# Optimization experiments

Measured on AMD Instinct MI355X. Metric: run time of the kernel, lower is better.

Reference implementation:

```python
import jax, jax.numpy as jnp
import numpy as np

N, C, H, W = 512, 512, 14, 14
CH, CW = 7, 7  # RoIAlign crop size


def conv1x1(x, w, b):
    # x: [N,C,H,W], w: [O,C], b: [O]  (1x1 conv == channel GEMM)
    return jnp.einsum('nchw,oc->nohw', x, w) + b[None, :, None, None]


def roi_align_fpcoor(x, boxes, ch, cw):
    """RoIAlign(transform_fpcoor=True) as in longcw/RoIAlign.pytorch.
    x: [N,C,H,W]; boxes: [N,4] = (x1,y1,x2,y2) in feature-pixel coords,
    box n crops image n. Returns [N,C,ch,cw]."""
    Hf, Wf = x.shape[2], x.shape[3]
    x1, y1, x2, y2 = boxes[:, 0], boxes[:, 1], boxes[:, 2], boxes[:, 3]
    sw = (x2 - x1) / cw
    sh = (y2 - y1) / ch
    nx0 = (x1 + sw * 0.5 - 0.5) / (Wf - 1)
    ny0 = (y1 + sh * 0.5 - 0.5) / (Hf - 1)
    nw = sw * (cw - 1) / (Wf - 1)
    nh = sh * (ch - 1) / (Hf - 1)
    # tf.crop_and_resize sample coordinates (crop size > 1 branch)
    ys = ny0[:, None] * (Hf - 1) + jnp.arange(ch, dtype=x.dtype) * (nh[:, None] * (Hf - 1) / (ch - 1))  # [N,ch]
    xs = nx0[:, None] * (Wf - 1) + jnp.arange(cw, dtype=x.dtype) * (nw[:, None] * (Wf - 1) / (cw - 1))  # [N,cw]
    y0f = jnp.floor(ys); x0f = jnp.floor(xs)
    wy = (ys - y0f)[:, :, None, None]          # [N,ch,1,1]
    wx = (xs - x0f)[:, None, :, None]          # [N,1,cw,1]
    y0 = jnp.clip(y0f.astype(jnp.int32), 0, Hf - 1)
    y1i = jnp.clip(y0 + 1, 0, Hf - 1)
    x0 = jnp.clip(x0f.astype(jnp.int32), 0, Wf - 1)
    x1i = jnp.clip(x0 + 1, 0, Wf - 1)
    b = jnp.arange(x.shape[0])[:, None, None]  # [N,1,1]
    yA = y0[:, :, None]; yB = y1i[:, :, None]  # [N,ch,1]
    xA = x0[:, None, :]; xB = x1i[:, None, :]  # [N,1,cw]
    # advanced indexing -> [N,ch,cw,C]
    v00 = x[b, :, yA, xA]; v01 = x[b, :, yA, xB]
    v10 = x[b, :, yB, xA]; v11 = x[b, :, yB, xB]
    top = v00 + (v01 - v00) * wx
    bot = v10 + (v11 - v10) * wx
    out = top + (bot - top) * wy               # [N,ch,cw,C]
    return jnp.transpose(out, (0, 3, 1, 2))    # [N,C,ch,cw]


def setup_inputs() -> dict:
    key = jax.random.key(0)
    ks = jax.random.split(key, 11)
    s = 0.02
    d = C * CH * CW  # 512*49
    return {
        'project': jax.random.normal(ks[0], (N, C, H, W), jnp.float32),
        'w1': jax.random.normal(ks[1], (C, C), jnp.float32) * s,
        'b1': jnp.zeros((C,), jnp.float32),
        'w2': jax.random.normal(ks[2], (C, C), jnp.float32) * s,
        'b2': jnp.zeros((C,), jnp.float32),
        'w3': jax.random.normal(ks[3], (C, C), jnp.float32) * s,
        'b3': jnp.zeros((C,), jnp.float32),
        'w_note': jax.random.normal(ks[4], (2, d), jnp.float32) * s,
        'b_note': jnp.zeros((2,), jnp.float32),
        'w_reg': jax.random.normal(ks[5], (8, d), jnp.float32) * s,
        'b_reg': jnp.zeros((8,), jnp.float32),
    }


def reference(project, w1, b1, w2, b2, w3, b3, w_note, b_note, w_reg, b_reg):
    x = conv1x1(project, w1, b1)
    x = conv1x1(x, w2, b2)
    # boxes are a fixed constant inside forward: [0,0,13,13] per RoI
    boxes = jnp.tile(jnp.asarray([[0.0, 0.0, 13.0, 13.0]], jnp.float32), (project.shape[0], 1))
    x = roi_align_fpcoor(x, boxes, CH, CW)     # [N,512,7,7]
    x = conv1x1(x, w3, b3)
    x = x.reshape((-1, C * CH * CW))
    note = x @ w_note.T + b_note
    reg = x @ w_reg.T + b_reg
    return note, reg
```

## Files before the change

### kernel.cpp

```cpp
#include <hip/hip_runtime.h>


#define CHW4 25088
#define STEP 1.8571428571428572f

__global__ __launch_bounds__(512) void k_prep1(
    const float* __restrict__ w_note, const float* __restrict__ w_reg,
    const float* __restrict__ w2, const float* __restrict__ b1,
    const float* __restrict__ b2,
    float* __restrict__ WH, float* __restrict__ u2) {
    int blk = blockIdx.x;
    int tid = threadIdx.x;
    if (blk < 490) {
        int k = blk / 49, ji = blk % 49;
        const float* wh = (k < 2) ? (w_note + k * 25088) : (w_reg + (k - 2) * 25088);
        WH[(size_t)blk * 512 + tid] = wh[tid * 49 + ji];
    } else {
        int wv = tid >> 6, lane = tid & 63;
        int o = (blk - 490) * 8 + wv;
        float s = 0.f;
        #pragma unroll
        for (int r = 0; r < 8; ++r) s += w2[(size_t)o * 512 + lane + r * 64] * b1[lane + r * 64];
        for (int off = 32; off; off >>= 1) s += __shfl_down(s, off);
        if (lane == 0) u2[o] = b2[o] + s;
    }
}

__global__ __launch_bounds__(256) void k_prep2(
    const float* __restrict__ w1, const float* __restrict__ w2,
    const float* __restrict__ w3, const float* __restrict__ WH,
    const float* __restrict__ u2, const float* __restrict__ b3,
    float* __restrict__ Y, float* __restrict__ T1, float* __restrict__ vv) {
    int blk = blockIdx.x;
    int tid = threadIdx.x;
    if (blk < 512) {
        __shared__ float As[32][36];
        __shared__ float Bs[32][36];
        const float* A; const float* B; float* C; int M;
        if (blk < 256) { A = w2; B = w1; C = Y;  M = 512; }
        else           { A = WH; B = w3; C = T1; M = 490; }
        int t = blk & 255;
        int bx = t & 15, by = t >> 4;
        int lr = tid >> 3, lc = (tid & 7) << 2;
        int tx = tid & 15, ty = tid >> 4;
        float a00 = 0.f, a01 = 0.f, a10 = 0.f, a11 = 0.f;
        for (int kc = 0; kc < 512; kc += 32) {
            int gr = by * 32 + lr;
            float4 av = make_float4(0.f, 0.f, 0.f, 0.f);
            if (gr < M) av = *(const float4*)&A[(size_t)gr * 512 + kc + lc];
            *(float4*)&As[lr][lc] = av;
            *(float4*)&Bs[lr][lc] = *(const float4*)&B[(size_t)(kc + lr) * 512 + bx * 32 + lc];
            __syncthreads();
            #pragma unroll
            for (int kk = 0; kk < 32; ++kk) {
                float b0 = Bs[kk][tx * 2], b1v = Bs[kk][tx * 2 + 1];
                float x0 = As[ty * 2][kk], x1 = As[ty * 2 + 1][kk];
                a00 += x0 * b0; a01 += x0 * b1v;
                a10 += x1 * b0; a11 += x1 * b1v;
            }
            __syncthreads();
        }
        int r0 = by * 32 + ty * 2, c0 = bx * 32 + tx * 2;
        if (r0 < M)     { C[(size_t)r0 * 512 + c0] = a00; C[(size_t)r0 * 512 + c0 + 1] = a01; }
        if (r0 + 1 < M) { C[(size_t)(r0 + 1) * 512 + c0] = a10; C[(size_t)(r0 + 1) * 512 + c0 + 1] = a11; }
    } else {
        int wv = tid >> 6, lane = tid & 63;
        int o = (blk - 512) * 4 + wv;
        float s = 0.f;
        #pragma unroll
        for (int r = 0; r < 8; ++r) s += w3[(size_t)o * 512 + lane + r * 64] * u2[lane + r * 64];
        for (int off = 32; off; off >>= 1) s += __shfl_down(s, off);
        if (lane == 0) vv[o] = b3[o] + s;
    }
}

__global__ __launch_bounds__(256) void k_prep3(
    const float* __restrict__ T1, const float* __restrict__ Y,
    const float* __restrict__ w_note, const float* __restrict__ w_reg,
    const float* __restrict__ vv,
    float* __restrict__ Bt, float* __restrict__ dpart) {
    int blk = blockIdx.x;
    int tid = threadIdx.x;
    if (blk < 256) {
        __shared__ float As[32][36];
        __shared__ float Bs[32][36];
        int bx = blk & 15, by = blk >> 4;
        int lr = tid >> 3, lc = (tid & 7) << 2;
        int tx = tid & 15, ty = tid >> 4;
        int gr = by * 32 + lr;
        float a00 = 0.f, a01 = 0.f, a10 = 0.f, a11 = 0.f;
        for (int kc = 0; kc < 512; kc += 32) {
            float4 av = make_float4(0.f, 0.f, 0.f, 0.f);
            if (gr < 490) av = *(const float4*)&T1[(size_t)gr * 512 + kc + lc];
            *(float4*)&As[lr][lc] = av;
            *(float4*)&Bs[lr][lc] = *(const float4*)&Y[(size_t)(kc + lr) * 512 + bx * 32 + lc];
            __syncthreads();
            #pragma unroll
            for (int kk = 0; kk < 32; ++kk) {
                float b0 = Bs[kk][tx * 2], b1v = Bs[kk][tx * 2 + 1];
                float x0 = As[ty * 2][kk], x1 = As[ty * 2 + 1][kk];
                a00 += x0 * b0; a01 += x0 * b1v;
                a10 += x1 * b0; a11 += x1 * b1v;
            }
            __syncthreads();
        }
        int r0 = by * 32 + ty * 2, c0 = bx * 32 + tx * 2;
        if (r0 < 490) {
            int k = r0 / 49, ji = r0 - k * 49;
            Bt[((size_t)(ji * 512 + c0)) * 12 + k] = a00;
            Bt[((size_t)(ji * 512 + c0 + 1)) * 12 + k] = a01;
        }
        if (r0 + 1 < 490) {
            int k = (r0 + 1) / 49, ji = (r0 + 1) - k * 49;
            Bt[((size_t)(ji * 512 + c0)) * 12 + k] = a10;
            Bt[((size_t)(ji * 512 + c0 + 1)) * 12 + k] = a11;
        }
    } else {
        int t = blk - 256;
        int k = t >> 3, b8 = t & 7;
        const float* wh = (k < 2) ? (w_note + k * 25088) : (w_reg + (k - 2) * 25088);
        float s = 0.f;
        for (int i = b8 * 256 + tid; i < 25088; i += 2048) s += wh[i] * vv[i / 49];
        __shared__ float red[256];
        red[tid] = s;
        __syncthreads();
        for (int off = 128; off; off >>= 1) {
            if (tid < off) red[tid] += red[tid + off];
            __syncthreads();
        }
        if (tid == 0) dpart[k * 8 + b8] = red[0];
    }
}

__global__ __launch_bounds__(256) void k_mainf(const float* __restrict__ proj,
                                               const float* __restrict__ Bt,
                                               float* __restrict__ part) {
    __shared__ float X[2][16][197];
    int b = blockIdx.x;
    int n = b >> 1;
    int ch0 = (b & 1) << 4;
    int tid = threadIdx.x;
    int wv = tid >> 6, lane = tid & 63;

    int cc0 = tid / 49,            q0 = tid - (tid / 49) * 49;
    int cc1 = cc0 + 5,             q1 = q0 + 11; if (q1 >= 49) { q1 -= 49; ++cc1; }
    int cc2 = cc1 + 5,             q2 = q1 + 11; if (q2 >= 49) { q2 -= 49; ++cc2; }

    const float base = STEP * 0.5f - 0.5f;
    int   i00s[4];
    float wxs[4], wys[4];
    size_t boff[4];
    #pragma unroll
    for (int s = 0; s < 4; ++s) {
        int o = tid + s * 256;
        if (o > 783) o = 783;
        int ji = o >> 4, cl = o & 15;
        int j = (ji * 37) >> 8;
        int i2 = ji - j * 7;
        float yv = base + j * STEP;
        float xv = base + i2 * STEP;
        float y0f = floorf(yv), x0f = floorf(xv);
        wys[s] = yv - y0f; wxs[s] = xv - x0f;
        i00s[s] = cl * 197 + (int)y0f * 14 + (int)x0f;
        boff[s] = ((size_t)(ji << 9) + (ch0 << 4) + cl) * 12;
    }

    const float4* src0 = (const float4*)proj + (size_t)n * CHW4 + ch0 * 784;
    float acc[10];
    #pragma unroll
    for (int k = 0; k < 10; ++k) acc[k] = 0.f;

    {
        float4 v0 = src0[tid];
        float4 v1 = src0[tid + 256];
        float4 v2 = src0[tid + 512];
        float* xb = &X[0][0][0];
        *(float4*)&xb[cc0 * 197 + q0 * 4] = v0;
        *(float4*)&xb[cc1 * 197 + q1 * 4] = v1;
        *(float4*)&xb[cc2 * 197 + q2 * 4] = v2;
        if (tid < 16) *(float4*)&xb[15 * 197 + (tid + 33) * 4] = src0[tid + 768];
    }
    __syncthreads();

    int cur = 0;
    #pragma unroll 1
    for (int t = 0; t < 16; ++t) {
        float4 v0, v1, v2, v3;
        if (t < 15) {
            const float4* sn = src0 + (t + 1) * 784;
            v0 = sn[tid]; v1 = sn[tid + 256]; v2 = sn[tid + 512];
            if (tid < 16) v3 = sn[tid + 768];
        }
        const float* xb = &X[cur][0][0];
        size_t tof = (size_t)t * 192;
        #pragma unroll
        for (int s = 0; s < 3; ++s) {
            int i00 = i00s[s];
            float v00 = xb[i00],      v01 = xb[i00 + 1];
            float v10 = xb[i00 + 14], v11 = xb[i00 + 15];
            float top = v00 + (v01 - v00) * wxs[s];
            float bot = v10 + (v11 - v10) * wxs[s];
            float v = top + (bot - top) * wys[s];
            const float* bp = Bt + boff[s] + tof;
            float4 c0 = *(const float4*)bp;
            float4 c1 = *(const float4*)(bp + 4);
            float2 c2 = *(const float2*)(bp + 8);
            acc[0] += v * c0.x; acc[1] += v * c0.y; acc[2] += v * c0.z; acc[3] += v * c0.w;
            acc[4] += v * c1.x; acc[5] += v * c1.y; acc[6] += v * c1.z; acc[7] += v * c1.w;
            acc[8] += v * c2.x; acc[9] += v * c2.y;
        }
        if (tid < 16) {
            int i00 = i00s[3];
            float v00 = xb[i00],      v01 = xb[i00 + 1];
            float v10 = xb[i00 + 14], v11 = xb[i00 + 15];
            float top = v00 + (v01 - v00) * wxs[3];
            float bot = v10 + (v11 - v10) * wxs[3];
            float v = top + (bot - top) * wys[3];
            const float* bp = Bt + boff[3] + tof;
            float4 c0 = *(const float4*)bp;
            float4 c1 = *(const float4*)(bp + 4);
            float2 c2 = *(const float2*)(bp + 8);
            acc[0] += v * c0.x; acc[1] += v * c0.y; acc[2] += v * c0.z; acc[3] += v * c0.w;
            acc[4] += v * c1.x; acc[5] += v * c1.y; acc[6] += v * c1.z; acc[7] += v * c1.w;
            acc[8] += v * c2.x; acc[9] += v * c2.y;
        }
        if (t < 15) {
            float* xw = &X[cur ^ 1][0][0];
            *(float4*)&xw[cc0 * 197 + q0 * 4] = v0;
            *(float4*)&xw[cc1 * 197 + q1 * 4] = v1;
            *(float4*)&xw[cc2 * 197 + q2 * 4] = v2;
            if (tid < 16) *(float4*)&xw[15 * 197 + (tid + 33) * 4] = v3;
        }
        __syncthreads();
        cur ^= 1;
    }

    #pragma unroll
    for (int k = 0; k < 10; ++k) {
        float v = acc[k];
        v += __shfl_xor(v, 1);
        v += __shfl_xor(v, 2);
        v += __shfl_xor(v, 4);
        v += __shfl_xor(v, 8);
        v += __shfl_xor(v, 16);
        v += __shfl_xor(v, 32);
        if (lane == k) part[((size_t)b * 4 + wv) * 10 + k] = v;
    }
}

__global__ void k_reduce(const float* __restrict__ part,
                         const float* __restrict__ dpart,
                         const float* __restrict__ b_note, const float* __restrict__ b_reg,
                         float* __restrict__ out) {
    int idx = blockIdx.x * 256 + threadIdx.x;
    int n = idx / 10, k = idx % 10;
    float s = (k < 2) ? b_note[k] : b_reg[k - 2];
    for (int b = 0; b < 8; ++b) s += dpart[k * 8 + b];
    #pragma unroll
    for (int h = 0; h < 2; ++h)
        for (int w = 0; w < 4; ++w)
            s += part[(((size_t)(n * 2 + h)) * 4 + w) * 10 + k];
    if (k < 2) out[n * 2 + k] = s;
    else       out[1024 + n * 8 + (k - 2)] = s;
}

extern "C" void kernel_launch(void* const* d_in, const int* in_sizes, int n_in,
                              void* d_out, int out_size, void* d_ws, size_t ws_size,
                              hipStream_t stream) {
    const float* proj   = (const float*)d_in[0];
    const float* w1     = (const float*)d_in[1];
    const float* b1     = (const float*)d_in[2];
    const float* w2     = (const float*)d_in[3];
    const float* b2     = (const float*)d_in[4];
    const float* w3     = (const float*)d_in[5];
    const float* b3     = (const float*)d_in[6];
    const float* w_note = (const float*)d_in[7];
    const float* b_note = (const float*)d_in[8];
    const float* w_reg  = (const float*)d_in[9];
    const float* b_reg  = (const float*)d_in[10];

    float* ws    = (float*)d_ws;
    float* WH    = ws;
    float* Y     = WH + 250880;
    float* T1    = Y + 262144;
    float* Bt    = T1 + 250880;
    float* u2    = Bt + 301056;
    float* vv    = u2 + 512;
    float* dpart = vv + 512;
    float* part  = dpart + 80;
    float* out   = (float*)d_out;

    k_prep1<<<554, 512, 0, stream>>>(w_note, w_reg, w2, b1, b2, WH, u2);
    k_prep2<<<640, 256, 0, stream>>>(w1, w2, w3, WH, u2, b3, Y, T1, vv);
    k_prep3<<<336, 256, 0, stream>>>(T1, Y, w_note, w_reg, vv, Bt, dpart);
    k_mainf<<<1024, 256, 0, stream>>>(proj, Bt, part);
    k_reduce<<<20, 256, 0, stream>>>(part, dpart, b_note, b_reg, out);
}
```

Measured before the change: 100.2 us.

## Give each wavefront its own 4-channel LDS tile and drop block barriers

Each of the four wavefronts now loads, stores to LDS and consumes its own 4-channel slice of the input, so no cross-wave sharing exists and the per-iteration __syncthreads is removed. Bt loads for all slots are issued at the top of each iteration, ahead of the next-tile prefetch, with a sched_barrier to fix that ordering and hide latency. This trades block-level synchronization for per-wave independence. It relies on LDS writes and reads within a wavefront being ordered without an explicit barrier, and it loads 12 floats per Bt slot where only 10 are used.

```diff
diff --git a/kernel.cpp b/kernel.cpp
--- a/kernel.cpp
+++ b/kernel.cpp
@@ -135,105 +135,106 @@
 __global__ __launch_bounds__(256) void k_mainf(const float* __restrict__ proj,
                                                const float* __restrict__ Bt,
                                                float* __restrict__ part) {
-    __shared__ float X[2][16][197];
+    __shared__ float X[4][2][788];
     int b = blockIdx.x;
     int n = b >> 1;
     int ch0 = (b & 1) << 4;
     int tid = threadIdx.x;
     int wv = tid >> 6, lane = tid & 63;
 
-    int cc0 = tid / 49,            q0 = tid - (tid / 49) * 49;
-    int cc1 = cc0 + 5,             q1 = q0 + 11; if (q1 >= 49) { q1 -= 49; ++cc1; }
-    int cc2 = cc1 + 5,             q2 = q1 + 11; if (q2 >= 49) { q2 -= 49; ++cc2; }
+    int cc0 = lane / 49, q0 = lane - cc0 * 49;
+    int cc1 = cc0 + 1, q1 = q0 + 15; if (q1 >= 49) { q1 -= 49; ++cc1; }
+    int cc2 = cc1 + 1, q2 = q1 + 15; if (q2 >= 49) { q2 -= 49; ++cc2; }
+    bool l4 = lane < 4;
+    int q3 = 45 + lane;
 
     const float base = STEP * 0.5f - 0.5f;
-    int   i00s[4];
+    int i00s[4], boffs[4];
     float wxs[4], wys[4];
-    size_t boff[4];
     #pragma unroll
     for (int s = 0; s < 4; ++s) {
-        int o = tid + s * 256;
-        if (o > 783) o = 783;
-        int ji = o >> 4, cl = o & 15;
+        int o = s * 64 + lane; if (o > 195) o = 195;
+        int ji = o >> 2, cl4 = o & 3;
         int j = (ji * 37) >> 8;
         int i2 = ji - j * 7;
         float yv = base + j * STEP;
         float xv = base + i2 * STEP;
         float y0f = floorf(yv), x0f = floorf(xv);
         wys[s] = yv - y0f; wxs[s] = xv - x0f;
-        i00s[s] = cl * 197 + (int)y0f * 14 + (int)x0f;
-        boff[s] = ((size_t)(ji << 9) + (ch0 << 4) + cl) * 12;
-    }
-
-    const float4* src0 = (const float4*)proj + (size_t)n * CHW4 + ch0 * 784;
+        i00s[s] = cl4 * 197 + (int)y0f * 14 + (int)x0f;
+        boffs[s] = ((ji << 9) + (ch0 << 4) + (wv << 2) + cl4) * 12;
+    }
+
+    const float4* srcb = (const float4*)proj + (size_t)n * CHW4 + ch0 * 784 + wv * 196;
     float acc[10];
     #pragma unroll
     for (int k = 0; k < 10; ++k) acc[k] = 0.f;
 
+    float4 v0, v1, v2, v3;
     {
-        float4 v0 = src0[tid];
-        float4 v1 = src0[tid + 256];
-        float4 v2 = src0[tid + 512];
-        float* xb = &X[0][0][0];
-        *(float4*)&xb[cc0 * 197 + q0 * 4] = v0;
-        *(float4*)&xb[cc1 * 197 + q1 * 4] = v1;
-        *(float4*)&xb[cc2 * 197 + q2 * 4] = v2;
-        if (tid < 16) *(float4*)&xb[15 * 197 + (tid + 33) * 4] = src0[tid + 768];
-    }
-    __syncthreads();
-
-    int cur = 0;
+        v0 = srcb[lane]; v1 = srcb[lane + 64]; v2 = srcb[lane + 128];
+        if (l4) v3 = srcb[lane + 192];
+        float* xw = &X[wv][0][0];
+        *(float4*)&xw[cc0 * 197 + q0 * 4] = v0;
+        *(float4*)&xw[cc1 * 197 + q1 * 4] = v1;
+        *(float4*)&xw[cc2 * 197 + q2 * 4] = v2;
+        if (l4) *(float4*)&xw[3 * 197 + q3 * 4] = v3;
+    }
+
+#define SLOT(S, Ca, Cb, Cc) do { \
+    int i00_ = i00s[S]; \
+    float v00 = xb[i00_],      v01 = xb[i00_ + 1]; \
+    float v10 = xb[i00_ + 14], v11 = xb[i00_ + 15]; \
+    float top = v00 + (v01 - v00) * wxs[S]; \
+    float bot = v10 + (v11 - v10) * wxs[S]; \
+    float v_ = top + (bot - top) * wys[S]; \
+    acc[0] += v_ * Ca.x; acc[1] += v_ * Ca.y; acc[2] += v_ * Ca.z; acc[3] += v_ * Ca.w; \
+    acc[4] += v_ * Cb.x; acc[5] += v_ * Cb.y; acc[6] += v_ * Cb.z; acc[7] += v_ * Cb.w; \
+    acc[8] += v_ * Cc.x; acc[9] += v_ * Cc.y; \
+} while (0)
+
     #pragma unroll 1
     for (int t = 0; t < 16; ++t) {
-        float4 v0, v1, v2, v3;
+        int tof = t * 192;
+        const float* bp0 = Bt + boffs[0] + tof;
+        float4 c00 = *(const float4*)bp0;
+        float4 c01 = *(const float4*)(bp0 + 4);
+        float4 c02 = *(const float4*)(bp0 + 8);
+        const float* bp1 = Bt + boffs[1] + tof;
+        float4 c10 = *(const float4*)bp1;
+        float4 c11 = *(const float4*)(bp1 + 4);
+        float4 c12 = *(const float4*)(bp1 + 8);
+        const float* bp2 = Bt + boffs[2] + tof;
+        float4 c20 = *(const float4*)bp2;
+        float4 c21 = *(const float4*)(bp2 + 4);
+        float4 c22 = *(const float4*)(bp2 + 8);
+        float4 c30, c31, c32;
+        if (l4) {
+            const float* bp3 = Bt + boffs[3] + tof;
+            c30 = *(const float4*)bp3;
+            c31 = *(const float4*)(bp3 + 4);
+            c32 = *(const float4*)(bp3 + 8);
+        }
         if (t < 15) {
-            const float4* sn = src0 + (t + 1) * 784;
-            v0 = sn[tid]; v1 = sn[tid + 256]; v2 = sn[tid + 512];
-            if (tid < 16) v3 = sn[tid + 768];
-        }
-        const float* xb = &X[cur][0][0];
-        size_t tof = (size_t)t * 192;
-        #pragma unroll
-        for (int s = 0; s < 3; ++s) {
-            int i00 = i00s[s];
-            float v00 = xb[i00],      v01 = xb[i00 + 1];
-            float v10 = xb[i00 + 14], v11 = xb[i00 + 15];
-            float top = v00 + (v01 - v00) * wxs[s];
-            float bot = v10 + (v11 - v10) * wxs[s];
-            float v = top + (bot - top) * wys[s];
-            const float* bp = Bt + boff[s] + tof;
-            float4 c0 = *(const float4*)bp;
-            float4 c1 = *(const float4*)(bp + 4);
-            float2 c2 = *(const float2*)(bp + 8);
-            acc[0] += v * c0.x; acc[1] += v * c0.y; acc[2] += v * c0.z; acc[3] += v * c0.w;
-            acc[4] += v * c1.x; acc[5] += v * c1.y; acc[6] += v * c1.z; acc[7] += v * c1.w;
-            acc[8] += v * c2.x; acc[9] += v * c2.y;
-        }
-        if (tid < 16) {
-            int i00 = i00s[3];
-            float v00 = xb[i00],      v01 = xb[i00 + 1];
-            float v10 = xb[i00 + 14], v11 = xb[i00 + 15];
-            float top = v00 + (v01 - v00) * wxs[3];
-            float bot = v10 + (v11 - v10) * wxs[3];
-            float v = top + (bot - top) * wys[3];
-            const float* bp = Bt + boff[3] + tof;
-            float4 c0 = *(const float4*)bp;
-            float4 c1 = *(const float4*)(bp + 4);
-            float2 c2 = *(const float2*)(bp + 8);
-            acc[0] += v * c0.x; acc[1] += v * c0.y; acc[2] += v * c0.z; acc[3] += v * c0.w;
-            acc[4] += v * c1.x; acc[5] += v * c1.y; acc[6] += v * c1.z; acc[7] += v * c1.w;
-            acc[8] += v * c2.x; acc[9] += v * c2.y;
-        }
+            const float4* sn = srcb + (t + 1) * 784;
+            v0 = sn[lane]; v1 = sn[lane + 64]; v2 = sn[lane + 128];
+            if (l4) v3 = sn[lane + 192];
+        }
+        __builtin_amdgcn_sched_barrier(0);
+        const float* xb = &X[wv][t & 1][0];
+        SLOT(0, c00, c01, c02);
+        SLOT(1, c10, c11, c12);
+        SLOT(2, c20, c21, c22);
+        if (l4) SLOT(3, c30, c31, c32);
         if (t < 15) {
-            float* xw = &X[cur ^ 1][0][0];
+            float* xw = &X[wv][(t + 1) & 1][0];
             *(float4*)&xw[cc0 * 197 + q0 * 4] = v0;
             *(float4*)&xw[cc1 * 197 + q1 * 4] = v1;
             *(float4*)&xw[cc2 * 197 + q2 * 4] = v2;
-            if (tid < 16) *(float4*)&xw[15 * 197 + (tid + 33) * 4] = v3;
-        }
-        __syncthreads();
-        cur ^= 1;
-    }
+            if (l4) *(float4*)&xw[3 * 197 + q3 * 4] = v3;
+        }
+    }
+#undef SLOT
 
     #pragma unroll
     for (int k = 0; k < 10; ++k) {
```

Result: slower. 103.0 us (+2.8%).
